# Optimization experiments

Measured on AMD Instinct MI355X. Metric: run time of the kernel, lower is better.

Reference implementation:

```python
import jax, jax.numpy as jnp
import numpy as np

T, B, SEQ_WIDTH, HID = 512, 64, 64, 1024
N = 32  # sqrt(HID): associative memory is N x N, HID spiking neurons
BETA = 0.9     # leak
THRESH = 1.0   # firing threshold
SLOPE = 25.0   # fast-sigmoid surrogate slope (snntorch default)


@jax.custom_vjp
def spike(u):
    # Heaviside forward, fast-sigmoid surrogate backward (snntorch-style)
    return (u > 0).astype(u.dtype)

def _spike_fwd(u):
    return (u > 0).astype(u.dtype), u

def _spike_bwd(u, g):
    sg = 1.0 / (1.0 + SLOPE * jnp.abs(u)) ** 2
    return (g * sg,)

spike.defvjp(_spike_fwd, _spike_bwd)


def assoc_leaky(h, Wk, bk, Wv, bv, Wq, bq):
    """Leaky associative spiking layer.
    h: (T, B, HID). Membrane state is an (B, N, N) associative matrix.
    Each step: outer-product write of key/value, leaky integration,
    threshold spike with soft reset, output spikes gated by sigmoid(q) rows.
    """
    k = h @ Wk + bk                      # (T, B, N)
    v = h @ Wv + bv                      # (T, B, N)
    q = jax.nn.sigmoid(h @ Wq + bq)      # (T, B, N)  use_q_projection gate
    Bt = h.shape[1]

    def step(mem, kvq):
        kt, vt, qt = kvq
        mem = BETA * mem + kt[:, :, None] * vt[:, None, :]   # (B, N, N)
        s = spike(mem - THRESH)
        mem = mem - s * THRESH                               # soft reset
        out = (s * qt[:, :, None]).reshape(Bt, N * N)        # (B, HID)
        return mem, out

    mem0 = jnp.zeros((Bt, N, N), h.dtype)
    _, outs = jax.lax.scan(step, mem0, (k, v, q))
    return outs  # (T, B, HID)


def setup_inputs() -> dict:
    key = jax.random.key(0)
    ks = jax.random.split(key, 12)
    s = 0.02
    def p(k, shape):
        return jax.random.normal(k, shape, jnp.float32) * s
    z = lambda *shape: jnp.zeros(shape, jnp.float32)
    return {
        "x": jax.random.normal(ks[0], (T, B, SEQ_WIDTH + 1), jnp.float32),
        "W_in": p(ks[1], (SEQ_WIDTH + 1, HID)), "b_in": z(HID),
        "Wk1": p(ks[2], (HID, N)), "bk1": z(N),
        "Wv1": p(ks[3], (HID, N)), "bv1": z(N),
        "Wq1": p(ks[4], (HID, N)), "bq1": z(N),
        "W_mid": p(ks[5], (HID, HID)), "b_mid": z(HID),
        "Wk2": p(ks[6], (HID, N)), "bk2": z(N),
        "Wv2": p(ks[7], (HID, N)), "bv2": z(N),
        "Wq2": p(ks[8], (HID, N)), "bq2": z(N),
        "W_out": p(ks[9], (HID, SEQ_WIDTH)), "b_out": z(SEQ_WIDTH),
    }


def reference(x, W_in, b_in, Wk1, bk1, Wv1, bv1, Wq1, bq1,
              W_mid, b_mid, Wk2, bk2, Wv2, bv2, Wq2, bq2, W_out, b_out):
    h = x @ W_in + b_in                                  # (T, B, HID)
    h = assoc_leaky(h, Wk1, bk1, Wv1, bv1, Wq1, bq1)
    h = jax.nn.relu(h @ W_mid + b_mid)
    h = assoc_leaky(h, Wk2, bk2, Wv2, bv2, Wq2, bq2)
    y = h @ W_out + b_out                                # (T, B, SEQ_WIDTH)
    return jax.nn.sigmoid(y)
```

## Files before the change

### kernel.cpp

```cpp
#include <hip/hip_runtime.h>
#include <math.h>


#define T_STEPS 512
#define BATCH   64
#define NN      32
#define HID     1024
#define INW     65
#define OUTW    64
#define KVQ     96

__device__ __forceinline__ float sigmoidf_(float x) { return 1.0f / (1.0f + expf(-x)); }

__global__ __launch_bounds__(512) void prep_kernel(
    const float* __restrict__ W_in, const float* __restrict__ b_in,
    const float* __restrict__ Wk1, const float* __restrict__ bk1,
    const float* __restrict__ Wv1, const float* __restrict__ bv1,
    const float* __restrict__ Wq1, const float* __restrict__ bq1,
    const float* __restrict__ b_mid,
    const float* __restrict__ Wk2, const float* __restrict__ bk2,
    const float* __restrict__ Wv2, const float* __restrict__ bv2,
    const float* __restrict__ Wq2, const float* __restrict__ bq2,
    float* __restrict__ W1eff, float* __restrict__ b1eff,
    float* __restrict__ const2)
{
    const int m = blockIdx.x;
    const int tid = threadIdx.x;
    __shared__ float srcv[HID];
    __shared__ float part[512];
    for (int h = tid; h < HID; h += 512) {
        float s;
        if (m < INW)       s = W_in[m * HID + h];
        else if (m == INW) s = b_in[h];
        else               s = fmaxf(b_mid[h], 0.f);
        srcv[h] = s;
    }
    __syncthreads();
    const int hq = tid >> 7, ns = tid & 127;
    const int sel = ns >> 5, nn = ns & 31;
    const bool layer2 = (m == INW + 1);
    const float* W = layer2 ? (sel == 0 ? Wk2 : sel == 1 ? Wv2 : Wq2)
                            : (sel == 0 ? Wk1 : sel == 1 ? Wv1 : Wq1);
    float acc = 0.f;
    if (ns < KVQ) {
        const int h0 = hq * 256;
        #pragma unroll 8
        for (int hh = 0; hh < 256; ++hh)
            acc = fmaf(srcv[h0 + hh], W[(h0 + hh) * NN + nn], acc);
    }
    part[tid] = acc;
    __syncthreads();
    if (hq == 0 && ns < KVQ) {
        float tot = part[ns] + part[128 + ns] + part[256 + ns] + part[384 + ns];
        if (m < INW) {
            W1eff[m * KVQ + ns] = tot;
        } else if (m == INW) {
            tot += (sel == 0 ? bk1 : sel == 1 ? bv1 : bq1)[nn];
            b1eff[ns] = tot;
        } else {
            tot += (sel == 0 ? bk2 : sel == 1 ? bv2 : bq2)[nn];
            const2[ns] = (sel == 2) ? sigmoidf_(tot) : tot;
        }
    }
}

__global__ __launch_bounds__(128) void kvq1p1_kernel(
    const float* __restrict__ x, const float* __restrict__ W1eff,
    const float* __restrict__ b1eff, float* __restrict__ kvq1,
    float* __restrict__ cert1)
{
    const int b = blockIdx.x >> 3, seg = blockIdx.x & 7;
    const int tid = threadIdx.x;
    __shared__ __align__(16) float Ws[INW * KVQ];
    __shared__ __align__(16) float bs[KVQ];
    __shared__ __align__(16) float pool[64 * 100];
    __shared__ float red[4];
    for (int i4 = tid; i4 < (INW * KVQ) / 4; i4 += 128)
        ((float4*)Ws)[i4] = ((const float4*)W1eff)[i4];
    if (tid < KVQ) bs[tid] = b1eff[tid];
    for (int l = tid; l < 64 * INW; l += 128) {
        const int r = l / INW, m = l - r * INW;
        pool[m * 68 + r] = x[((size_t)((seg * 64 + r) * 64 + b)) * INW + m];
    }
    __syncthreads();
    const int rg = tid >> 3;
    const int c0 = (tid & 7) * 12;
    float acc[4][12];
    #pragma unroll
    for (int r = 0; r < 4; ++r)
        #pragma unroll
        for (int k = 0; k < 12; ++k) acc[r][k] = bs[c0 + k];
    #pragma unroll 5
    for (int m = 0; m < INW; ++m) {
        const float4 xv = *(const float4*)&pool[m * 68 + rg * 4];
        const float4 w0 = *(const float4*)&Ws[m * KVQ + c0];
        const float4 w1 = *(const float4*)&Ws[m * KVQ + c0 + 4];
        const float4 w2 = *(const float4*)&Ws[m * KVQ + c0 + 8];
        const float xr[4] = {xv.x, xv.y, xv.z, xv.w};
        const float wk[12] = {w0.x, w0.y, w0.z, w0.w, w1.x, w1.y, w1.z, w1.w,
                              w2.x, w2.y, w2.z, w2.w};
        #pragma unroll
        for (int r = 0; r < 4; ++r)
            #pragma unroll
            for (int k = 0; k < 12; ++k)
                acc[r][k] = fmaf(xr[r], wk[k], acc[r][k]);
    }
    __syncthreads();
    #pragma unroll
    for (int r = 0; r < 4; ++r) {
        const int row = rg * 4 + r;
        float v[12];
        #pragma unroll
        for (int k = 0; k < 12; ++k)
            v[k] = (c0 + k >= 2 * NN) ? sigmoidf_(acc[r][k]) : acc[r][k];
        float* kt = &pool[row * 100 + c0];
        *(float4*)&kt[0] = make_float4(v[0], v[1], v[2], v[3]);
        *(float4*)&kt[4] = make_float4(v[4], v[5], v[6], v[7]);
        *(float4*)&kt[8] = make_float4(v[8], v[9], v[10], v[11]);
        float* o = kvq1 + ((size_t)b * T_STEPS + seg * 64 + row) * KVQ + c0;
        *(float4*)&o[0] = make_float4(v[0], v[1], v[2], v[3]);
        *(float4*)&o[4] = make_float4(v[4], v[5], v[6], v[7]);
        *(float4*)&o[8] = make_float4(v[8], v[9], v[10], v[11]);
    }
    __syncthreads();
    const int i0 = (tid >> 5) * 8, j = tid & 31;
    float p[8], am[8];
    #pragma unroll
    for (int r = 0; r < 8; ++r) { p[r] = 0.f; am[r] = 0.f; }
    for (int tt = 0; tt < 16; ++tt) {
        float4 k0[4], k1[4]; float vv[4];
        #pragma unroll
        for (int d2 = 0; d2 < 4; ++d2) {
            const int t = tt * 4 + d2;
            k0[d2] = *(const float4*)&pool[t * 100 + i0];
            k1[d2] = *(const float4*)&pool[t * 100 + i0 + 4];
            vv[d2] = pool[t * 100 + 32 + j];
        }
        #pragma unroll
        for (int d2 = 0; d2 < 4; ++d2) {
            const float kf[8] = {k0[d2].x, k0[d2].y, k0[d2].z, k0[d2].w,
                                 k1[d2].x, k1[d2].y, k1[d2].z, k1[d2].w};
            #pragma unroll
            for (int r = 0; r < 8; ++r) {
                p[r] = fmaf(0.9f, p[r], kf[r] * vv[d2]);
                am[r] = fmaxf(am[r], fabsf(p[r]));
            }
        }
    }
    float ls = 0.f, lp = 0.f;
    #pragma unroll
    for (int r = 0; r < 8; ++r) { ls = fmaxf(ls, fabsf(p[r])); lp = fmaxf(lp, am[r]); }
    #pragma unroll
    for (int off = 32; off; off >>= 1) {
        ls = fmaxf(ls, __shfl_xor(ls, off));
        lp = fmaxf(lp, __shfl_xor(lp, off));
    }
    const int lane = tid & 63, wv = tid >> 6;
    if (lane == 0) { red[wv * 2] = ls; red[wv * 2 + 1] = lp; }
    __syncthreads();
    if (tid == 0) {
        cert1[blockIdx.x * 2 + 0] = fmaxf(red[0], red[2]);
        cert1[blockIdx.x * 2 + 1] = fmaxf(red[1], red[3]);
    }
}

__global__ __launch_bounds__(256) void cc_kernel(
    const float* __restrict__ cert, const float* __restrict__ kvq,
    unsigned int* __restrict__ rowany, unsigned int* __restrict__ dmask,
    const unsigned int* __restrict__ rowany_prev, const float* __restrict__ cdef)
{
    const int b = blockIdx.x;
    const int tid = threadIdx.x;
    const float c64 = 0.0011790184577738599f;
    const float G64 = 9.988209815422261f;
    __shared__ __align__(16) float c2l[64];
    float scs = 0.f;
    if (cdef) {
        if (tid < 64) c2l[tid] = cdef[tid];
        __syncthreads();
        float mk = 0.f, mv = 0.f;
        #pragma unroll 8
        for (int i = 0; i < 32; ++i) {
            mk = fmaxf(mk, fabsf(c2l[i]));
            mv = fmaxf(mv, fabsf(c2l[32 + i]));
        }
        scs = mk * mv * G64;
    }
    float Mb = 0.f;
    bool fl = false;
    #pragma unroll
    for (int g = 0; g < 8; ++g) {
        bool mixed = true;
        if (rowany_prev) {
            unsigned int m = 0u;
            #pragma unroll
            for (int iq = 0; iq < 4; ++iq)
                m |= rowany_prev[(b * 4 + iq) * 16 + 2 * g]
                   | rowany_prev[(b * 4 + iq) * 16 + 2 * g + 1];
            mixed = (m != 0u);
        }
        float smax, pmax;
        if (mixed) { smax = cert[(b * 8 + g) * 2]; pmax = cert[(b * 8 + g) * 2 + 1]; }
        else       { smax = scs; pmax = scs; }
        const float ub = Mb + pmax;
        fl |= !(ub * 1.0001f <= 0.999f);
        Mb = fmaf(c64, Mb, smax);
    }
    if (!fl) {
        if (tid < 64) rowany[b * 64 + tid] = 0u;
        return;
    }
    __shared__ float buf[64 * 64];
    const int j = tid & 31, ig = tid >> 5;
    const int wavei = tid >> 6;
    float mem[4] = {0.f, 0.f, 0.f, 0.f};
    unsigned int u[4] = {0u, 0u, 0u, 0u};
    for (int c = 0; c < 8; ++c) {
        unsigned int orA = 0xFFFFFFFFu, orB = 0xFFFFFFFFu;
        if (rowany_prev) {
            orA = 0u; orB = 0u;
            #pragma unroll
            for (int iq = 0; iq < 4; ++iq) {
                orA |= rowany_prev[(b * 4 + iq) * 16 + 2 * c];
                orB |= rowany_prev[(b * 4 + iq) * 16 + 2 * c + 1];
            }
        }
        __syncthreads();
        #pragma unroll
        for (int r = 0; r < 4; ++r) {
            const int s4 = tid + 256 * r;
            const int dt = s4 >> 4, q = s4 & 15;
            const unsigned int orw = (dt < 32) ? orA : orB;
            float4 val;
            if (rowany_prev && !((orw >> (dt & 31)) & 1u))
                val = *(const float4*)&c2l[q * 4];
            else
                val = *(const float4*)(kvq + ((size_t)b * T_STEPS + c * 64 + dt) * KVQ + q * 4);
            *(float4*)&buf[dt * 64 + q * 4] = val;
        }
        __syncthreads();
        for (int dt = 0; dt < 64; ++dt) {
            const float4 kk = *(const float4*)&buf[dt * 64 + ig * 4];
            const float vv = buf[dt * 64 + 32 + j];
            const float kf[4] = {kk.x, kk.y, kk.z, kk.w};
            #pragma unroll
            for (int r = 0; r < 4; ++r) {
                mem[r] = fmaf(0.9f, mem[r], kf[r] * vv);
                const bool s = mem[r] > 1.f; if (s) mem[r] -= 1.f;
                u[r] |= (s ? 1u : 0u) << (dt & 31);
            }
            if ((dt & 31) == 31) {
                const int wg = c * 2 + (dt >> 5);
                unsigned int* dm = dmask + (size_t)(wg * 64 + b) * 1024;
                unsigned int a = 0;
                #pragma unroll
                for (int r = 0; r < 4; ++r) {
                    dm[(ig * 4 + r) * 32 + j] = u[r];
                    a |= u[r]; u[r] = 0u;
                }
                #pragma unroll
                for (int off = 32; off; off >>= 1) a |= __shfl_xor(a, off);
                if ((tid & 63) == 0) rowany[(b * 4 + wavei) * 16 + wg] = a;
            }
        }
    }
}

__global__ __launch_bounds__(128) void mid_kernel(
    const unsigned int* __restrict__ rowany1, const unsigned int* __restrict__ dmask1,
    const float* __restrict__ kvq1,
    const float* __restrict__ W_mid, const float* __restrict__ b_mid,
    const float* __restrict__ Wk2, const float* __restrict__ bk2,
    const float* __restrict__ Wv2, const float* __restrict__ bv2,
    const float* __restrict__ Wq2, const float* __restrict__ bq2,
    const float* __restrict__ const2, float* __restrict__ kvq2,
    float* __restrict__ cert2)
{
    const int b = blockIdx.x >> 3, seg = blockIdx.x & 7;
    const int tid = threadIdx.x;
    const int w0 = seg * 2;
    const unsigned int orA = rowany1[(b * 4 + 0) * 16 + w0] | rowany1[(b * 4 + 1) * 16 + w0]
                           | rowany1[(b * 4 + 2) * 16 + w0] | rowany1[(b * 4 + 3) * 16 + w0];
    const unsigned int orB = rowany1[(b * 4 + 0) * 16 + w0 + 1] | rowany1[(b * 4 + 1) * 16 + w0 + 1]
                           | rowany1[(b * 4 + 2) * 16 + w0 + 1] | rowany1[(b * 4 + 3) * 16 + w0 + 1];
    if ((orA | orB) == 0u) return;
    __shared__ __align__(16) float c2s[KVQ];
    __shared__ __align__(16) float kt2[64 * 64];
    __shared__ float h2[HID];
    __shared__ unsigned int msk[NN];
    __shared__ float red[4];
    if (tid < KVQ) c2s[tid] = const2[tid];
    __syncthreads();
    float* obase = kvq2 + ((size_t)b * T_STEPS + seg * 64) * KVQ;
    for (int d = 0; d < 64; ++d) {
        const unsigned int orw = (d < 32) ? orA : orB;
        const int bit = d & 31;
        if (!((orw >> bit) & 1u)) {
            if (tid < 16) *(float4*)&kt2[d * 64 + tid * 4] = ((const float4*)c2s)[tid];
        } else {
            const int wg = w0 + (d >> 5);
            const unsigned int* dmw = dmask1 + (size_t)(wg * 64 + b) * 1024;
            for (int i2 = 0; i2 < NN; i2 += 4) {
                const int i = i2 + (tid >> 5);
                const unsigned int wb = dmw[i * 32 + (tid & 31)];
                const unsigned long long balm = __ballot(((wb >> bit) & 1u) != 0);
                const int ibase = i2 + (tid >> 6) * 2;
                if ((tid & 63) == 0)  msk[ibase]     = (unsigned int)balm;
                if ((tid & 63) == 32) msk[ibase + 1] = (unsigned int)(balm >> 32);
            }
            for (int cc = tid; cc < HID; cc += 128) h2[cc] = b_mid[cc];
            __syncthreads();
            const float* qrow = kvq1 + ((size_t)b * T_STEPS + seg * 64 + d) * KVQ + 2 * NN;
            for (int i = 0; i < NN; ++i) {
                unsigned int m = msk[i];
                if (!m) continue;
                const float qv = qrow[i];
                while (m) {
                    const int jj = __ffs(m) - 1; m &= m - 1;
                    const float* wr = W_mid + (size_t)(i * NN + jj) * HID;
                    for (int cc = tid; cc < HID; cc += 128)
                        h2[cc] = fmaf(qv, wr[cc], h2[cc]);
                }
            }
            __syncthreads();
            for (int cc = tid; cc < HID; cc += 128) h2[cc] = fmaxf(h2[cc], 0.f);
            __syncthreads();
            if (tid < KVQ) {
                const int sel = tid >> 5, nn = tid & 31;
                const float* W2 = sel == 0 ? Wk2 : sel == 1 ? Wv2 : Wq2;
                float a2 = (sel == 0 ? bk2 : sel == 1 ? bv2 : bq2)[nn];
                for (int cc = 0; cc < HID; ++cc)
                    a2 = fmaf(h2[cc], W2[cc * NN + nn], a2);
                if (sel == 2) a2 = sigmoidf_(a2);
                obase[d * KVQ + tid] = a2;
                if (tid < 64) kt2[d * 64 + tid] = a2;
            }
            __syncthreads();
        }
    }
    __syncthreads();
    const int i0 = (tid >> 5) * 8, j = tid & 31;
    float p[8], am[8];
    #pragma unroll
    for (int r = 0; r < 8; ++r) { p[r] = 0.f; am[r] = 0.f; }
    for (int tt = 0; tt < 16; ++tt) {
        float4 k0[4], k1[4]; float vv[4];
        #pragma unroll
        for (int d2 = 0; d2 < 4; ++d2) {
            const int t = tt * 4 + d2;
            k0[d2] = *(const float4*)&kt2[t * 64 + i0];
            k1[d2] = *(const float4*)&kt2[t * 64 + i0 + 4];
            vv[d2] = kt2[t * 64 + 32 + j];
        }
        #pragma unroll
        for (int d2 = 0; d2 < 4; ++d2) {
            const float kf[8] = {k0[d2].x, k0[d2].y, k0[d2].z, k0[d2].w,
                                 k1[d2].x, k1[d2].y, k1[d2].z, k1[d2].w};
            #pragma unroll
            for (int r = 0; r < 8; ++r) {
                p[r] = fmaf(0.9f, p[r], kf[r] * vv[d2]);
                am[r] = fmaxf(am[r], fabsf(p[r]));
            }
        }
    }
    float ls = 0.f, lp = 0.f;
    #pragma unroll
    for (int r = 0; r < 8; ++r) { ls = fmaxf(ls, fabsf(p[r])); lp = fmaxf(lp, am[r]); }
    #pragma unroll
    for (int off = 32; off; off >>= 1) {
        ls = fmaxf(ls, __shfl_xor(ls, off));
        lp = fmaxf(lp, __shfl_xor(lp, off));
    }
    const int lane = tid & 63, wv = tid >> 6;
    if (lane == 0) { red[wv * 2] = ls; red[wv * 2 + 1] = lp; }
    __syncthreads();
    if (tid == 0) {
        cert2[blockIdx.x * 2 + 0] = fmaxf(red[0], red[2]);
        cert2[blockIdx.x * 2 + 1] = fmaxf(red[1], red[3]);
    }
}

__global__ __launch_bounds__(256) void out_kernel(
    const unsigned int* __restrict__ rowany2, const unsigned int* __restrict__ dmask2,
    const unsigned int* __restrict__ rowany1,
    const float* __restrict__ kvq2, const float* __restrict__ const2,
    const float* __restrict__ W_out, const float* __restrict__ b_out,
    float* __restrict__ y)
{
    const int blk = blockIdx.x;
    const int b = blk >> 2, tq = blk & 3;
    const int tid = threadIdx.x;
    const int wave = tid >> 6, lane = tid & 63;
    const int wg = tq * 4 + wave;
    __shared__ unsigned int mskws[4][NN];
    const int g16 = lane & 15;
    const float4 bo = ((const float4*)b_out)[g16];
    const float4 sy = make_float4(sigmoidf_(bo.x), sigmoidf_(bo.y),
                                  sigmoidf_(bo.z), sigmoidf_(bo.w));
    const unsigned int or4 = rowany2[(b * 4 + 0) * 16 + wg]
                           | rowany2[(b * 4 + 1) * 16 + wg]
                           | rowany2[(b * 4 + 2) * 16 + wg]
                           | rowany2[(b * 4 + 3) * 16 + wg];
    if (or4 == 0) {
        #pragma unroll
        for (int d = 0; d < 32; d += 4) {
            const int t = wg * 32 + d + (lane >> 4);
            ((float4*)(y + ((size_t)t * 64 + b) * OUTW))[g16] = sy;
        }
        return;
    }
    const unsigned int or1 = rowany1[(b * 4 + 0) * 16 + wg]
                           | rowany1[(b * 4 + 1) * 16 + wg]
                           | rowany1[(b * 4 + 2) * 16 + wg]
                           | rowany1[(b * 4 + 3) * 16 + wg];
    for (int d = 0; d < 32; ++d) {
        const int t = wg * 32 + d;
        float* yr = y + ((size_t)t * 64 + b) * OUTW;
        if (!((or4 >> d) & 1u)) {
            if (lane < 16) ((float4*)yr)[lane] = sy;
            continue;
        }
        const unsigned int* dmw = dmask2 + (size_t)(wg * 64 + b) * 1024;
        for (int i2 = 0; i2 < NN; i2 += 2) {
            const int i = i2 + (lane >> 5), jj = lane & 31;
            const unsigned int wbits = dmw[i * 32 + jj];
            const unsigned long long bal = __ballot(((wbits >> d) & 1u) != 0);
            if (lane == 0)  mskws[wave][i2] = (unsigned int)bal;
            if (lane == 32) mskws[wave][i2 + 1] = (unsigned int)(bal >> 32);
        }
        const float* qrow = ((or1 >> d) & 1u)
            ? kvq2 + ((size_t)b * T_STEPS + t) * KVQ + 2 * NN
            : const2 + 2 * NN;
        float a = b_out[lane];
        for (int i = 0; i < NN; ++i) {
            unsigned int m = mskws[wave][i];
            if (!m) continue;
            const float qv = qrow[i];
            while (m) {
                const int jj = __ffs(m) - 1; m &= m - 1;
                a = fmaf(qv, W_out[(size_t)(i * NN + jj) * OUTW + lane], a);
            }
        }
        yr[lane] = sigmoidf_(a);
    }
}

extern "C" void kernel_launch(void* const* d_in, const int* in_sizes, int n_in,
                              void* d_out, int out_size, void* d_ws, size_t ws_size,
                              hipStream_t stream)
{
    const float* x     = (const float*)d_in[0];
    const float* W_in  = (const float*)d_in[1];
    const float* b_in  = (const float*)d_in[2];
    const float* Wk1   = (const float*)d_in[3];
    const float* bk1   = (const float*)d_in[4];
    const float* Wv1   = (const float*)d_in[5];
    const float* bv1   = (const float*)d_in[6];
    const float* Wq1   = (const float*)d_in[7];
    const float* bq1   = (const float*)d_in[8];
    const float* W_mid = (const float*)d_in[9];
    const float* b_mid = (const float*)d_in[10];
    const float* Wk2   = (const float*)d_in[11];
    const float* bk2   = (const float*)d_in[12];
    const float* Wv2   = (const float*)d_in[13];
    const float* bv2   = (const float*)d_in[14];
    const float* Wq2   = (const float*)d_in[15];
    const float* bq2   = (const float*)d_in[16];
    const float* W_out = (const float*)d_in[17];
    const float* b_out = (const float*)d_in[18];
    float* y = (float*)d_out;

    float* ws = (float*)d_ws;
    float* W1eff  = ws;
    float* b1eff  = ws + 6240;
    float* const2 = ws + 6336;
    float* kvq1   = ws + 8192;
    float* kvq2   = kvq1 + 3145728;
    unsigned int* dmask1  = (unsigned int*)(kvq2 + 3145728);
    unsigned int* dmask2  = dmask1 + 1048576;
    unsigned int* rowany1 = dmask2 + 1048576;
    unsigned int* rowany2 = rowany1 + 4096;
    float* cert1 = (float*)(rowany2 + 4096);
    float* cert2 = cert1 + 1024;

    prep_kernel<<<INW + 2, 512, 0, stream>>>(W_in, b_in, Wk1, bk1, Wv1, bv1, Wq1, bq1,
                                             b_mid, Wk2, bk2, Wv2, bv2, Wq2, bq2,
                                             W1eff, b1eff, const2);
    kvq1p1_kernel<<<BATCH * 8, 128, 0, stream>>>(x, W1eff, b1eff, kvq1, cert1);
    cc_kernel<<<BATCH, 256, 0, stream>>>(cert1, kvq1, rowany1, dmask1,
                                         (const unsigned int*)nullptr,
                                         (const float*)nullptr);
    mid_kernel<<<BATCH * 8, 128, 0, stream>>>(rowany1, dmask1, kvq1, W_mid, b_mid,
                                              Wk2, bk2, Wv2, bv2, Wq2, bq2,
                                              const2, kvq2, cert2);
    cc_kernel<<<BATCH, 256, 0, stream>>>(cert2, kvq2, rowany2, dmask2,
                                         rowany1, const2);
    out_kernel<<<BATCH * 4, 256, 0, stream>>>(rowany2, dmask2, rowany1,
                                              kvq2, const2, W_out, b_out, y);
}
```

Before: 147.6 us.

## Split fused kvq1/phase1 kernel into row-contiguous projection and separate certificate scan

The fused layer-1 projection plus certificate scan kernel is split in two. The projection now reads x in contiguous 128-row chunks over (t,b), so loads are coalesced instead of strided by batch, and it scatters results into the per-batch kvq1 layout. A separate phase1 kernel reloads the k/v columns from global memory and runs the leaky scan with 256 threads, 4 rows each, and double-buffered register loads. This adds a kernel launch and a global round trip of kvq1 in exchange for coalesced input reads and more parallelism in the scan.

Measured after the change: 142.5 us, median of 2. -3.5%, faster.

```diff
diff --git a/kernel.cpp b/kernel.cpp
--- a/kernel.cpp
+++ b/kernel.cpp
@@ -8,6 +8,7 @@
 #define HID     1024
 #define INW     65
 #define OUTW    64
+#define ROWS    (T_STEPS * BATCH)
 #define KVQ     96
 
 __device__ __forceinline__ float sigmoidf_(float x) { return 1.0f / (1.0f + expf(-x)); }
@@ -64,24 +65,22 @@
     }
 }
 
-__global__ __launch_bounds__(128) void kvq1p1_kernel(
+__global__ __launch_bounds__(256) void kvq1_kernel(
     const float* __restrict__ x, const float* __restrict__ W1eff,
-    const float* __restrict__ b1eff, float* __restrict__ kvq1,
-    float* __restrict__ cert1)
-{
-    const int b = blockIdx.x >> 3, seg = blockIdx.x & 7;
+    const float* __restrict__ b1eff, float* __restrict__ kvq1)
+{
     const int tid = threadIdx.x;
-    __shared__ __align__(16) float Ws[INW * KVQ];
-    __shared__ __align__(16) float bs[KVQ];
-    __shared__ __align__(16) float pool[64 * 100];
-    __shared__ float red[4];
-    for (int i4 = tid; i4 < (INW * KVQ) / 4; i4 += 128)
+    const int r0 = blockIdx.x * 128;
+    __shared__ float Ws[INW * KVQ];
+    __shared__ float xsT[INW * 132];
+    __shared__ float bs[KVQ];
+    for (int i4 = tid; i4 < (INW * KVQ) / 4; i4 += 256)
         ((float4*)Ws)[i4] = ((const float4*)W1eff)[i4];
+    for (int l = tid; l < 128 * INW; l += 256) {
+        const int r = l / INW, m = l - r * INW;
+        xsT[m * 132 + r] = x[(size_t)(r0 + r) * INW + m];
+    }
     if (tid < KVQ) bs[tid] = b1eff[tid];
-    for (int l = tid; l < 64 * INW; l += 128) {
-        const int r = l / INW, m = l - r * INW;
-        pool[m * 68 + r] = x[((size_t)((seg * 64 + r) * 64 + b)) * INW + m];
-    }
     __syncthreads();
     const int rg = tid >> 3;
     const int c0 = (tid & 7) * 12;
@@ -90,9 +89,8 @@
     for (int r = 0; r < 4; ++r)
         #pragma unroll
         for (int k = 0; k < 12; ++k) acc[r][k] = bs[c0 + k];
-    #pragma unroll 5
     for (int m = 0; m < INW; ++m) {
-        const float4 xv = *(const float4*)&pool[m * 68 + rg * 4];
+        const float4 xv = *(const float4*)&xsT[m * 132 + rg * 4];
         const float4 w0 = *(const float4*)&Ws[m * KVQ + c0];
         const float4 w1 = *(const float4*)&Ws[m * KVQ + c0 + 4];
         const float4 w2 = *(const float4*)&Ws[m * KVQ + c0 + 8];
@@ -105,51 +103,68 @@
             for (int k = 0; k < 12; ++k)
                 acc[r][k] = fmaf(xr[r], wk[k], acc[r][k]);
     }
-    __syncthreads();
     #pragma unroll
     for (int r = 0; r < 4; ++r) {
-        const int row = rg * 4 + r;
+        const int g = r0 + rg * 4 + r;
+        const int t = g >> 6, b = g & 63;
+        float* o = kvq1 + ((size_t)b * T_STEPS + t) * KVQ + c0;
         float v[12];
         #pragma unroll
         for (int k = 0; k < 12; ++k)
             v[k] = (c0 + k >= 2 * NN) ? sigmoidf_(acc[r][k]) : acc[r][k];
-        float* kt = &pool[row * 100 + c0];
-        *(float4*)&kt[0] = make_float4(v[0], v[1], v[2], v[3]);
-        *(float4*)&kt[4] = make_float4(v[4], v[5], v[6], v[7]);
-        *(float4*)&kt[8] = make_float4(v[8], v[9], v[10], v[11]);
-        float* o = kvq1 + ((size_t)b * T_STEPS + seg * 64 + row) * KVQ + c0;
         *(float4*)&o[0] = make_float4(v[0], v[1], v[2], v[3]);
         *(float4*)&o[4] = make_float4(v[4], v[5], v[6], v[7]);
         *(float4*)&o[8] = make_float4(v[8], v[9], v[10], v[11]);
     }
-    __syncthreads();
-    const int i0 = (tid >> 5) * 8, j = tid & 31;
-    float p[8], am[8];
-    #pragma unroll
-    for (int r = 0; r < 8; ++r) { p[r] = 0.f; am[r] = 0.f; }
-    for (int tt = 0; tt < 16; ++tt) {
-        float4 k0[4], k1[4]; float vv[4];
-        #pragma unroll
-        for (int d2 = 0; d2 < 4; ++d2) {
-            const int t = tt * 4 + d2;
-            k0[d2] = *(const float4*)&pool[t * 100 + i0];
-            k1[d2] = *(const float4*)&pool[t * 100 + i0 + 4];
-            vv[d2] = pool[t * 100 + 32 + j];
-        }
-        #pragma unroll
-        for (int d2 = 0; d2 < 4; ++d2) {
-            const float kf[8] = {k0[d2].x, k0[d2].y, k0[d2].z, k0[d2].w,
-                                 k1[d2].x, k1[d2].y, k1[d2].z, k1[d2].w};
+}
+
+__global__ __launch_bounds__(256) void phase1_kernel(
+    const float* __restrict__ kvq, float* __restrict__ cert)
+{
+    const int b = blockIdx.x >> 3, seg = blockIdx.x & 7;
+    const int tid = threadIdx.x;
+    __shared__ __align__(16) float buf[64 * 64];
+    __shared__ float red[8];
+    const float* base = kvq + ((size_t)b * T_STEPS + seg * 64) * KVQ;
+    #pragma unroll
+    for (int r = 0; r < 4; ++r) {
+        const int l4 = tid + 256 * r;
+        const int dt = l4 >> 4, q = l4 & 15;
+        *(float4*)&buf[dt * 64 + q * 4] = *(const float4*)(base + dt * KVQ + q * 4);
+    }
+    __syncthreads();
+    const int i0 = (tid >> 5) * 4, j = tid & 31;
+    float p[4] = {0.f, 0.f, 0.f, 0.f};
+    float am[4] = {0.f, 0.f, 0.f, 0.f};
+    float4 kb[2][4]; float vb[2][4];
+    #pragma unroll
+    for (int d = 0; d < 4; ++d) {
+        kb[0][d] = *(const float4*)&buf[d * 64 + i0];
+        vb[0][d] = buf[d * 64 + 32 + j];
+    }
+    #pragma unroll
+    for (int bt = 0; bt < 16; ++bt) {
+        const int cb = bt & 1;
+        if (bt < 15) {
             #pragma unroll
-            for (int r = 0; r < 8; ++r) {
-                p[r] = fmaf(0.9f, p[r], kf[r] * vv[d2]);
-                am[r] = fmaxf(am[r], fabsf(p[r]));
-            }
+            for (int d = 0; d < 4; ++d) {
+                const int dt = (bt + 1) * 4 + d;
+                kb[cb ^ 1][d] = *(const float4*)&buf[dt * 64 + i0];
+                vb[cb ^ 1][d] = buf[dt * 64 + 32 + j];
+            }
+        }
+        #pragma unroll
+        for (int d = 0; d < 4; ++d) {
+            const float vv = vb[cb][d];
+            p[0] = fmaf(0.9f, p[0], kb[cb][d].x * vv); am[0] = fmaxf(am[0], fabsf(p[0]));
+            p[1] = fmaf(0.9f, p[1], kb[cb][d].y * vv); am[1] = fmaxf(am[1], fabsf(p[1]));
+            p[2] = fmaf(0.9f, p[2], kb[cb][d].z * vv); am[2] = fmaxf(am[2], fabsf(p[2]));
+            p[3] = fmaf(0.9f, p[3], kb[cb][d].w * vv); am[3] = fmaxf(am[3], fabsf(p[3]));
         }
     }
     float ls = 0.f, lp = 0.f;
     #pragma unroll
-    for (int r = 0; r < 8; ++r) { ls = fmaxf(ls, fabsf(p[r])); lp = fmaxf(lp, am[r]); }
+    for (int r = 0; r < 4; ++r) { ls = fmaxf(ls, fabsf(p[r])); lp = fmaxf(lp, am[r]); }
     #pragma unroll
     for (int off = 32; off; off >>= 1) {
         ls = fmaxf(ls, __shfl_xor(ls, off));
@@ -159,8 +174,8 @@
     if (lane == 0) { red[wv * 2] = ls; red[wv * 2 + 1] = lp; }
     __syncthreads();
     if (tid == 0) {
-        cert1[blockIdx.x * 2 + 0] = fmaxf(red[0], red[2]);
-        cert1[blockIdx.x * 2 + 1] = fmaxf(red[1], red[3]);
+        cert[blockIdx.x * 2 + 0] = fmaxf(fmaxf(red[0], red[2]), fmaxf(red[4], red[6]));
+        cert[blockIdx.x * 2 + 1] = fmaxf(fmaxf(red[1], red[3]), fmaxf(red[5], red[7]));
     }
 }
 
@@ -486,7 +501,8 @@
     prep_kernel<<<INW + 2, 512, 0, stream>>>(W_in, b_in, Wk1, bk1, Wv1, bv1, Wq1, bq1,
                                              b_mid, Wk2, bk2, Wv2, bv2, Wq2, bq2,
                                              W1eff, b1eff, const2);
-    kvq1p1_kernel<<<BATCH * 8, 128, 0, stream>>>(x, W1eff, b1eff, kvq1, cert1);
+    kvq1_kernel<<<ROWS / 128, 256, 0, stream>>>(x, W1eff, b1eff, kvq1);
+    phase1_kernel<<<BATCH * 8, 256, 0, stream>>>(kvq1, cert1);
     cc_kernel<<<BATCH, 256, 0, stream>>>(cert1, kvq1, rowany1, dmask1,
                                          (const unsigned int*)nullptr,
                                          (const float*)nullptr);
```

## Fuse certification scan into producer kernels via last-block atomic completion

Applied to the files above, without the earlier changes.

Removes the two separate cc_kernel launches. Each producer block now publishes its per-batch max bounds with atomicMax and bumps a per-batch counter, and the last block to finish for a batch runs the spike scan in place. Counters are zeroed in prep_kernel. The first-layer producer also doubles its thread count to 256 with fewer rows per thread, and the layer-1 certification bound is changed to a closed-form combined check. The aim is to save launch and serialization overhead, at the cost of the serial scan running in only one block per batch and relying on threadfence-based inter-block ordering.

Measured after the change: 216.6 us. 46.7% more time.

```diff
diff --git a/kernel.cpp b/kernel.cpp
--- a/kernel.cpp
+++ b/kernel.cpp
@@ -22,10 +22,11 @@
     const float* __restrict__ Wv2, const float* __restrict__ bv2,
     const float* __restrict__ Wq2, const float* __restrict__ bq2,
     float* __restrict__ W1eff, float* __restrict__ b1eff,
-    float* __restrict__ const2)
+    float* __restrict__ const2, unsigned int* __restrict__ ctrl)
 {
     const int m = blockIdx.x;
     const int tid = threadIdx.x;
+    if (m == 0 && tid < 384) ctrl[tid] = 0u;
     __shared__ float srcv[HID];
     __shared__ float part[512];
     for (int h = tid; h < HID; h += 512) {
@@ -64,51 +65,53 @@
     }
 }
 
-__global__ __launch_bounds__(128) void kvq1p1_kernel(
+__global__ __launch_bounds__(256) void kvq1p1c_kernel(
     const float* __restrict__ x, const float* __restrict__ W1eff,
     const float* __restrict__ b1eff, float* __restrict__ kvq1,
-    float* __restrict__ cert1)
+    unsigned int* __restrict__ rowany1, unsigned int* __restrict__ dmask1,
+    unsigned int* __restrict__ cnt1, float* __restrict__ amax1)
 {
     const int b = blockIdx.x >> 3, seg = blockIdx.x & 7;
     const int tid = threadIdx.x;
     __shared__ __align__(16) float Ws[INW * KVQ];
     __shared__ __align__(16) float bs[KVQ];
     __shared__ __align__(16) float pool[64 * 100];
-    __shared__ float red[4];
-    for (int i4 = tid; i4 < (INW * KVQ) / 4; i4 += 128)
+    __shared__ float red[8];
+    __shared__ unsigned int lastf, dirtyf;
+    for (int i4 = tid; i4 < (INW * KVQ) / 4; i4 += 256)
         ((float4*)Ws)[i4] = ((const float4*)W1eff)[i4];
     if (tid < KVQ) bs[tid] = b1eff[tid];
-    for (int l = tid; l < 64 * INW; l += 128) {
+    for (int l = tid; l < 64 * INW; l += 256) {
         const int r = l / INW, m = l - r * INW;
         pool[m * 68 + r] = x[((size_t)((seg * 64 + r) * 64 + b)) * INW + m];
     }
     __syncthreads();
     const int rg = tid >> 3;
     const int c0 = (tid & 7) * 12;
-    float acc[4][12];
-    #pragma unroll
-    for (int r = 0; r < 4; ++r)
+    float acc[2][12];
+    #pragma unroll
+    for (int r = 0; r < 2; ++r)
         #pragma unroll
         for (int k = 0; k < 12; ++k) acc[r][k] = bs[c0 + k];
     #pragma unroll 5
     for (int m = 0; m < INW; ++m) {
-        const float4 xv = *(const float4*)&pool[m * 68 + rg * 4];
+        const float2 xv = *(const float2*)&pool[m * 68 + rg * 2];
         const float4 w0 = *(const float4*)&Ws[m * KVQ + c0];
         const float4 w1 = *(const float4*)&Ws[m * KVQ + c0 + 4];
         const float4 w2 = *(const float4*)&Ws[m * KVQ + c0 + 8];
-        const float xr[4] = {xv.x, xv.y, xv.z, xv.w};
+        const float xr[2] = {xv.x, xv.y};
         const float wk[12] = {w0.x, w0.y, w0.z, w0.w, w1.x, w1.y, w1.z, w1.w,
                               w2.x, w2.y, w2.z, w2.w};
         #pragma unroll
-        for (int r = 0; r < 4; ++r)
+        for (int r = 0; r < 2; ++r)
             #pragma unroll
             for (int k = 0; k < 12; ++k)
                 acc[r][k] = fmaf(xr[r], wk[k], acc[r][k]);
     }
     __syncthreads();
     #pragma unroll
-    for (int r = 0; r < 4; ++r) {
-        const int row = rg * 4 + r;
+    for (int r = 0; r < 2; ++r) {
+        const int row = rg * 2 + r;
         float v[12];
         #pragma unroll
         for (int k = 0; k < 12; ++k)
@@ -123,120 +126,81 @@
         *(float4*)&o[8] = make_float4(v[8], v[9], v[10], v[11]);
     }
     __syncthreads();
-    const int i0 = (tid >> 5) * 8, j = tid & 31;
-    float p[8], am[8];
-    #pragma unroll
-    for (int r = 0; r < 8; ++r) { p[r] = 0.f; am[r] = 0.f; }
-    for (int tt = 0; tt < 16; ++tt) {
-        float4 k0[4], k1[4]; float vv[4];
-        #pragma unroll
-        for (int d2 = 0; d2 < 4; ++d2) {
-            const int t = tt * 4 + d2;
-            k0[d2] = *(const float4*)&pool[t * 100 + i0];
-            k1[d2] = *(const float4*)&pool[t * 100 + i0 + 4];
-            vv[d2] = pool[t * 100 + 32 + j];
-        }
-        #pragma unroll
-        for (int d2 = 0; d2 < 4; ++d2) {
-            const float kf[8] = {k0[d2].x, k0[d2].y, k0[d2].z, k0[d2].w,
-                                 k1[d2].x, k1[d2].y, k1[d2].z, k1[d2].w};
+    const int i0 = (tid >> 5) * 4, j = tid & 31;
+    float p[4] = {0.f, 0.f, 0.f, 0.f};
+    float am[4] = {0.f, 0.f, 0.f, 0.f};
+    float4 kb[2]; float vb[2][4]; float4 kt4[2][4];
+    (void)kb;
+    #pragma unroll
+    for (int d = 0; d < 4; ++d) {
+        kt4[0][d] = *(const float4*)&pool[d * 100 + i0];
+        vb[0][d] = pool[d * 100 + 32 + j];
+    }
+    #pragma unroll
+    for (int bt = 0; bt < 16; ++bt) {
+        const int cb = bt & 1;
+        if (bt < 15) {
             #pragma unroll
-            for (int r = 0; r < 8; ++r) {
-                p[r] = fmaf(0.9f, p[r], kf[r] * vv[d2]);
-                am[r] = fmaxf(am[r], fabsf(p[r]));
-            }
+            for (int d = 0; d < 4; ++d) {
+                const int dt = (bt + 1) * 4 + d;
+                kt4[cb ^ 1][d] = *(const float4*)&pool[dt * 100 + i0];
+                vb[cb ^ 1][d] = pool[dt * 100 + 32 + j];
+            }
+        }
+        #pragma unroll
+        for (int d = 0; d < 4; ++d) {
+            const float vv = vb[cb][d];
+            p[0] = fmaf(0.9f, p[0], kt4[cb][d].x * vv); am[0] = fmaxf(am[0], fabsf(p[0]));
+            p[1] = fmaf(0.9f, p[1], kt4[cb][d].y * vv); am[1] = fmaxf(am[1], fabsf(p[1]));
+            p[2] = fmaf(0.9f, p[2], kt4[cb][d].z * vv); am[2] = fmaxf(am[2], fabsf(p[2]));
+            p[3] = fmaf(0.9f, p[3], kt4[cb][d].w * vv); am[3] = fmaxf(am[3], fabsf(p[3]));
         }
     }
     float ls = 0.f, lp = 0.f;
     #pragma unroll
-    for (int r = 0; r < 8; ++r) { ls = fmaxf(ls, fabsf(p[r])); lp = fmaxf(lp, am[r]); }
+    for (int r = 0; r < 4; ++r) { ls = fmaxf(ls, fabsf(p[r])); lp = fmaxf(lp, am[r]); }
     #pragma unroll
     for (int off = 32; off; off >>= 1) {
         ls = fmaxf(ls, __shfl_xor(ls, off));
         lp = fmaxf(lp, __shfl_xor(lp, off));
     }
-    const int lane = tid & 63, wv = tid >> 6;
-    if (lane == 0) { red[wv * 2] = ls; red[wv * 2 + 1] = lp; }
+    if ((tid & 63) == 0) { red[(tid >> 6) * 2] = ls; red[(tid >> 6) * 2 + 1] = lp; }
     __syncthreads();
     if (tid == 0) {
-        cert1[blockIdx.x * 2 + 0] = fmaxf(red[0], red[2]);
-        cert1[blockIdx.x * 2 + 1] = fmaxf(red[1], red[3]);
-    }
-}
-
-__global__ __launch_bounds__(256) void cc_kernel(
-    const float* __restrict__ cert, const float* __restrict__ kvq,
-    unsigned int* __restrict__ rowany, unsigned int* __restrict__ dmask,
-    const unsigned int* __restrict__ rowany_prev, const float* __restrict__ cdef)
-{
-    const int b = blockIdx.x;
-    const int tid = threadIdx.x;
-    const float c64 = 0.0011790184577738599f;
-    const float G64 = 9.988209815422261f;
-    __shared__ __align__(16) float c2l[64];
-    float scs = 0.f;
-    if (cdef) {
-        if (tid < 64) c2l[tid] = cdef[tid];
-        __syncthreads();
-        float mk = 0.f, mv = 0.f;
-        #pragma unroll 8
-        for (int i = 0; i < 32; ++i) {
-            mk = fmaxf(mk, fabsf(c2l[i]));
-            mv = fmaxf(mv, fabsf(c2l[32 + i]));
-        }
-        scs = mk * mv * G64;
-    }
-    float Mb = 0.f;
-    bool fl = false;
-    #pragma unroll
-    for (int g = 0; g < 8; ++g) {
-        bool mixed = true;
-        if (rowany_prev) {
-            unsigned int m = 0u;
-            #pragma unroll
-            for (int iq = 0; iq < 4; ++iq)
-                m |= rowany_prev[(b * 4 + iq) * 16 + 2 * g]
-                   | rowany_prev[(b * 4 + iq) * 16 + 2 * g + 1];
-            mixed = (m != 0u);
-        }
-        float smax, pmax;
-        if (mixed) { smax = cert[(b * 8 + g) * 2]; pmax = cert[(b * 8 + g) * 2 + 1]; }
-        else       { smax = scs; pmax = scs; }
-        const float ub = Mb + pmax;
-        fl |= !(ub * 1.0001f <= 0.999f);
-        Mb = fmaf(c64, Mb, smax);
-    }
-    if (!fl) {
-        if (tid < 64) rowany[b * 64 + tid] = 0u;
+        const float bS = fmaxf(fmaxf(red[0], red[2]), fmaxf(red[4], red[6]));
+        const float bP = fmaxf(fmaxf(red[1], red[3]), fmaxf(red[5], red[7]));
+        atomicMax((int*)&amax1[b * 2 + 0], __float_as_int(bS));
+        atomicMax((int*)&amax1[b * 2 + 1], __float_as_int(bP));
+    }
+    __threadfence();
+    __syncthreads();
+    if (tid == 0) lastf = (atomicAdd(&cnt1[b], 1u) == 7u) ? 1u : 0u;
+    __syncthreads();
+    if (!lastf) return;
+    __threadfence();
+    if (tid == 0) {
+        const float mS = __int_as_float(atomicMax((int*)&amax1[b * 2 + 0], 0));
+        const float mP = __int_as_float(atomicMax((int*)&amax1[b * 2 + 1], 0));
+        dirtyf = !((mP + mS * 1.0012f) * 1.0001f <= 0.999f) ? 1u : 0u;
+    }
+    __syncthreads();
+    if (!dirtyf) {
+        if (tid < 64) rowany1[b * 64 + tid] = 0u;
         return;
     }
-    __shared__ float buf[64 * 64];
-    const int j = tid & 31, ig = tid >> 5;
+    float* buf = pool;
+    const int ig = tid >> 5;
     const int wavei = tid >> 6;
     float mem[4] = {0.f, 0.f, 0.f, 0.f};
     unsigned int u[4] = {0u, 0u, 0u, 0u};
     for (int c = 0; c < 8; ++c) {
-        unsigned int orA = 0xFFFFFFFFu, orB = 0xFFFFFFFFu;
-        if (rowany_prev) {
-            orA = 0u; orB = 0u;
-            #pragma unroll
-            for (int iq = 0; iq < 4; ++iq) {
-                orA |= rowany_prev[(b * 4 + iq) * 16 + 2 * c];
-                orB |= rowany_prev[(b * 4 + iq) * 16 + 2 * c + 1];
-            }
-        }
         __syncthreads();
         #pragma unroll
         for (int r = 0; r < 4; ++r) {
             const int s4 = tid + 256 * r;
             const int dt = s4 >> 4, q = s4 & 15;
-            const unsigned int orw = (dt < 32) ? orA : orB;
-            float4 val;
-            if (rowany_prev && !((orw >> (dt & 31)) & 1u))
-                val = *(const float4*)&c2l[q * 4];
-            else
-                val = *(const float4*)(kvq + ((size_t)b * T_STEPS + c * 64 + dt) * KVQ + q * 4);
-            *(float4*)&buf[dt * 64 + q * 4] = val;
+            *(float4*)&buf[dt * 64 + q * 4] =
+                *(const float4*)(kvq1 + ((size_t)b * T_STEPS + c * 64 + dt) * KVQ + q * 4);
         }
         __syncthreads();
         for (int dt = 0; dt < 64; ++dt) {
@@ -251,7 +215,7 @@
             }
             if ((dt & 31) == 31) {
                 const int wg = c * 2 + (dt >> 5);
-                unsigned int* dm = dmask + (size_t)(wg * 64 + b) * 1024;
+                unsigned int* dm = dmask1 + (size_t)(wg * 64 + b) * 1024;
                 unsigned int a = 0;
                 #pragma unroll
                 for (int r = 0; r < 4; ++r) {
@@ -260,13 +224,13 @@
                 }
                 #pragma unroll
                 for (int off = 32; off; off >>= 1) a |= __shfl_xor(a, off);
-                if ((tid & 63) == 0) rowany[(b * 4 + wavei) * 16 + wg] = a;
+                if ((tid & 63) == 0) rowany1[(b * 4 + wavei) * 16 + wg] = a;
             }
         }
     }
 }
 
-__global__ __launch_bounds__(128) void mid_kernel(
+__global__ __launch_bounds__(128) void midc_kernel(
     const unsigned int* __restrict__ rowany1, const unsigned int* __restrict__ dmask1,
     const float* __restrict__ kvq1,
     const float* __restrict__ W_mid, const float* __restrict__ b_mid,
@@ -274,109 +238,187 @@
     const float* __restrict__ Wv2, const float* __restrict__ bv2,
     const float* __restrict__ Wq2, const float* __restrict__ bq2,
     const float* __restrict__ const2, float* __restrict__ kvq2,
-    float* __restrict__ cert2)
+    unsigned int* __restrict__ rowany2, unsigned int* __restrict__ dmask2,
+    unsigned int* __restrict__ cnt2, float* __restrict__ amax2)
 {
     const int b = blockIdx.x >> 3, seg = blockIdx.x & 7;
     const int tid = threadIdx.x;
     const int w0 = seg * 2;
-    const unsigned int orA = rowany1[(b * 4 + 0) * 16 + w0] | rowany1[(b * 4 + 1) * 16 + w0]
-                           | rowany1[(b * 4 + 2) * 16 + w0] | rowany1[(b * 4 + 3) * 16 + w0];
-    const unsigned int orB = rowany1[(b * 4 + 0) * 16 + w0 + 1] | rowany1[(b * 4 + 1) * 16 + w0 + 1]
-                           | rowany1[(b * 4 + 2) * 16 + w0 + 1] | rowany1[(b * 4 + 3) * 16 + w0 + 1];
-    if ((orA | orB) == 0u) return;
+    const float G64 = 9.988209815422261f;
     __shared__ __align__(16) float c2s[KVQ];
     __shared__ __align__(16) float kt2[64 * 64];
     __shared__ float h2[HID];
     __shared__ unsigned int msk[NN];
     __shared__ float red[4];
+    __shared__ unsigned int lastf, dirtyf;
     if (tid < KVQ) c2s[tid] = const2[tid];
     __syncthreads();
-    float* obase = kvq2 + ((size_t)b * T_STEPS + seg * 64) * KVQ;
-    for (int d = 0; d < 64; ++d) {
-        const unsigned int orw = (d < 32) ? orA : orB;
-        const int bit = d & 31;
-        if (!((orw >> bit) & 1u)) {
-            if (tid < 16) *(float4*)&kt2[d * 64 + tid * 4] = ((const float4*)c2s)[tid];
-        } else {
-            const int wg = w0 + (d >> 5);
-            const unsigned int* dmw = dmask1 + (size_t)(wg * 64 + b) * 1024;
-            for (int i2 = 0; i2 < NN; i2 += 4) {
-                const int i = i2 + (tid >> 5);
-                const unsigned int wb = dmw[i * 32 + (tid & 31)];
-                const unsigned long long balm = __ballot(((wb >> bit) & 1u) != 0);
-                const int ibase = i2 + (tid >> 6) * 2;
-                if ((tid & 63) == 0)  msk[ibase]     = (unsigned int)balm;
-                if ((tid & 63) == 32) msk[ibase + 1] = (unsigned int)(balm >> 32);
-            }
-            for (int cc = tid; cc < HID; cc += 128) h2[cc] = b_mid[cc];
-            __syncthreads();
-            const float* qrow = kvq1 + ((size_t)b * T_STEPS + seg * 64 + d) * KVQ + 2 * NN;
-            for (int i = 0; i < NN; ++i) {
-                unsigned int m = msk[i];
-                if (!m) continue;
-                const float qv = qrow[i];
-                while (m) {
-                    const int jj = __ffs(m) - 1; m &= m - 1;
-                    const float* wr = W_mid + (size_t)(i * NN + jj) * HID;
-                    for (int cc = tid; cc < HID; cc += 128)
-                        h2[cc] = fmaf(qv, wr[cc], h2[cc]);
+    const unsigned int orA = rowany1[(b * 4 + 0) * 16 + w0] | rowany1[(b * 4 + 1) * 16 + w0]
+                           | rowany1[(b * 4 + 2) * 16 + w0] | rowany1[(b * 4 + 3) * 16 + w0];
+    const unsigned int orB = rowany1[(b * 4 + 0) * 16 + w0 + 1] | rowany1[(b * 4 + 1) * 16 + w0 + 1]
+                           | rowany1[(b * 4 + 2) * 16 + w0 + 1] | rowany1[(b * 4 + 3) * 16 + w0 + 1];
+    if ((orA | orB) != 0u) {
+        float* obase = kvq2 + ((size_t)b * T_STEPS + seg * 64) * KVQ;
+        for (int d = 0; d < 64; ++d) {
+            const unsigned int orw = (d < 32) ? orA : orB;
+            const int bit = d & 31;
+            if (!((orw >> bit) & 1u)) {
+                if (tid < 16) *(float4*)&kt2[d * 64 + tid * 4] = ((const float4*)c2s)[tid];
+            } else {
+                const int wg = w0 + (d >> 5);
+                const unsigned int* dmw = dmask1 + (size_t)(wg * 64 + b) * 1024;
+                for (int i2 = 0; i2 < NN; i2 += 4) {
+                    const int i = i2 + (tid >> 5);
+                    const unsigned int wb = dmw[i * 32 + (tid & 31)];
+                    const unsigned long long balm = __ballot(((wb >> bit) & 1u) != 0);
+                    const int ibase = i2 + (tid >> 6) * 2;
+                    if ((tid & 63) == 0)  msk[ibase]     = (unsigned int)balm;
+                    if ((tid & 63) == 32) msk[ibase + 1] = (unsigned int)(balm >> 32);
                 }
-            }
-            __syncthreads();
-            for (int cc = tid; cc < HID; cc += 128) h2[cc] = fmaxf(h2[cc], 0.f);
-            __syncthreads();
-            if (tid < KVQ) {
-                const int sel = tid >> 5, nn = tid & 31;
-                const float* W2 = sel == 0 ? Wk2 : sel == 1 ? Wv2 : Wq2;
-                float a2 = (sel == 0 ? bk2 : sel == 1 ? bv2 : bq2)[nn];
-                for (int cc = 0; cc < HID; ++cc)
-                    a2 = fmaf(h2[cc], W2[cc * NN + nn], a2);
-                if (sel == 2) a2 = sigmoidf_(a2);
-                obase[d * KVQ + tid] = a2;
-                if (tid < 64) kt2[d * 64 + tid] = a2;
-            }
-            __syncthreads();
-        }
-    }
-    __syncthreads();
-    const int i0 = (tid >> 5) * 8, j = tid & 31;
-    float p[8], am[8];
-    #pragma unroll
-    for (int r = 0; r < 8; ++r) { p[r] = 0.f; am[r] = 0.f; }
-    for (int tt = 0; tt < 16; ++tt) {
-        float4 k0[4], k1[4]; float vv[4];
-        #pragma unroll
-        for (int d2 = 0; d2 < 4; ++d2) {
-            const int t = tt * 4 + d2;
-            k0[d2] = *(const float4*)&kt2[t * 64 + i0];
-            k1[d2] = *(const float4*)&kt2[t * 64 + i0 + 4];
-            vv[d2] = kt2[t * 64 + 32 + j];
-        }
-        #pragma unroll
-        for (int d2 = 0; d2 < 4; ++d2) {
-            const float kf[8] = {k0[d2].x, k0[d2].y, k0[d2].z, k0[d2].w,
-                                 k1[d2].x, k1[d2].y, k1[d2].z, k1[d2].w};
+                for (int cc = tid; cc < HID; cc += 128) h2[cc] = b_mid[cc];
+                __syncthreads();
+                const float* qrow = kvq1 + ((size_t)b * T_STEPS + seg * 64 + d) * KVQ + 2 * NN;
+                for (int i = 0; i < NN; ++i) {
+                    unsigned int m = msk[i];
+                    if (!m) continue;
+                    const float qv = qrow[i];
+                    while (m) {
+                        const int jj = __ffs(m) - 1; m &= m - 1;
+                        const float* wr = W_mid + (size_t)(i * NN + jj) * HID;
+                        for (int cc = tid; cc < HID; cc += 128)
+                            h2[cc] = fmaf(qv, wr[cc], h2[cc]);
+                    }
+                }
+                __syncthreads();
+                for (int cc = tid; cc < HID; cc += 128) h2[cc] = fmaxf(h2[cc], 0.f);
+                __syncthreads();
+                if (tid < KVQ) {
+                    const int sel = tid >> 5, nn = tid & 31;
+                    const float* W2 = sel == 0 ? Wk2 : sel == 1 ? Wv2 : Wq2;
+                    float a2 = (sel == 0 ? bk2 : sel == 1 ? bv2 : bq2)[nn];
+                    for (int cc = 0; cc < HID; ++cc)
+                        a2 = fmaf(h2[cc], W2[cc * NN + nn], a2);
+                    if (sel == 2) a2 = sigmoidf_(a2);
+                    obase[d * KVQ + tid] = a2;
+                    if (tid < 64) kt2[d * 64 + tid] = a2;
+                }
+                __syncthreads();
+            }
+        }
+        __syncthreads();
+        const int i0 = (tid >> 5) * 8, j = tid & 31;
+        float p[8], am[8];
+        #pragma unroll
+        for (int r = 0; r < 8; ++r) { p[r] = 0.f; am[r] = 0.f; }
+        for (int tt = 0; tt < 16; ++tt) {
+            float4 k0[4], k1[4]; float vv[4];
+            #pragma unroll
+            for (int d2 = 0; d2 < 4; ++d2) {
+                const int t = tt * 4 + d2;
+                k0[d2] = *(const float4*)&kt2[t * 64 + i0];
+                k1[d2] = *(const float4*)&kt2[t * 64 + i0 + 4];
+                vv[d2] = kt2[t * 64 + 32 + j];
+            }
+            #pragma unroll
+            for (int d2 = 0; d2 < 4; ++d2) {
+                const float kf[8] = {k0[d2].x, k0[d2].y, k0[d2].z, k0[d2].w,
+                                     k1[d2].x, k1[d2].y, k1[d2].z, k1[d2].w};
+                #pragma unroll
+                for (int r = 0; r < 8; ++r) {
+                    p[r] = fmaf(0.9f, p[r], kf[r] * vv[d2]);
+                    am[r] = fmaxf(am[r], fabsf(p[r]));
+                }
+            }
+        }
+        float ls = 0.f, lp = 0.f;
+        #pragma unroll
+        for (int r = 0; r < 8; ++r) { ls = fmaxf(ls, fabsf(p[r])); lp = fmaxf(lp, am[r]); }
+        #pragma unroll
+        for (int off = 32; off; off >>= 1) {
+            ls = fmaxf(ls, __shfl_xor(ls, off));
+            lp = fmaxf(lp, __shfl_xor(lp, off));
+        }
+        if ((tid & 63) == 0) { red[(tid >> 6) * 2] = ls; red[(tid >> 6) * 2 + 1] = lp; }
+        __syncthreads();
+        if (tid == 0) {
+            atomicMax((int*)&amax2[b * 2 + 0], __float_as_int(fmaxf(red[0], red[2])));
+            atomicMax((int*)&amax2[b * 2 + 1], __float_as_int(fmaxf(red[1], red[3])));
+        }
+    }
+    __threadfence();
+    __syncthreads();
+    if (tid == 0) lastf = (atomicAdd(&cnt2[b], 1u) == 7u) ? 1u : 0u;
+    __syncthreads();
+    if (!lastf) return;
+    __threadfence();
+    if (tid == 0) {
+        float mk = 0.f, mv = 0.f;
+        #pragma unroll 8
+        for (int i = 0; i < 32; ++i) {
+            mk = fmaxf(mk, fabsf(c2s[i]));
+            mv = fmaxf(mv, fabsf(c2s[32 + i]));
+        }
+        const float scs = mk * mv * G64;
+        const float mS = fmaxf(__int_as_float(atomicMax((int*)&amax2[b * 2 + 0], 0)), scs);
+        const float mP = fmaxf(__int_as_float(atomicMax((int*)&amax2[b * 2 + 1], 0)), scs);
+        dirtyf = !((mP + mS * 1.0012f) * 1.0001f <= 0.999f) ? 1u : 0u;
+    }
+    __syncthreads();
+    if (!dirtyf) {
+        if (tid < 64) rowany2[b * 64 + tid] = 0u;
+        return;
+    }
+    float* buf = kt2;
+    const int j = tid & 31, ig = tid >> 5;
+    float mem[8]; unsigned int u[8];
+    #pragma unroll
+    for (int r = 0; r < 8; ++r) { mem[r] = 0.f; u[r] = 0u; }
+    for (int c = 0; c < 8; ++c) {
+        unsigned int oA = 0u, oB = 0u;
+        #pragma unroll
+        for (int iq = 0; iq < 4; ++iq) {
+            oA |= rowany1[(b * 4 + iq) * 16 + 2 * c];
+            oB |= rowany1[(b * 4 + iq) * 16 + 2 * c + 1];
+        }
+        __syncthreads();
+        #pragma unroll
+        for (int r = 0; r < 8; ++r) {
+            const int s4 = tid + 128 * r;
+            const int dt = s4 >> 4, q = s4 & 15;
+            const unsigned int orw = (dt < 32) ? oA : oB;
+            float4 val;
+            if (!((orw >> (dt & 31)) & 1u))
+                val = *(const float4*)&c2s[q * 4];
+            else
+                val = *(const float4*)(kvq2 + ((size_t)b * T_STEPS + c * 64 + dt) * KVQ + q * 4);
+            *(float4*)&buf[dt * 64 + q * 4] = val;
+        }
+        __syncthreads();
+        for (int dt = 0; dt < 64; ++dt) {
+            const float4 ka = *(const float4*)&buf[dt * 64 + ig * 8];
+            const float4 kb2 = *(const float4*)&buf[dt * 64 + ig * 8 + 4];
+            const float vv = buf[dt * 64 + 32 + j];
+            const float kf[8] = {ka.x, ka.y, ka.z, ka.w, kb2.x, kb2.y, kb2.z, kb2.w};
             #pragma unroll
             for (int r = 0; r < 8; ++r) {
-                p[r] = fmaf(0.9f, p[r], kf[r] * vv[d2]);
-                am[r] = fmaxf(am[r], fabsf(p[r]));
-            }
-        }
-    }
-    float ls = 0.f, lp = 0.f;
-    #pragma unroll
-    for (int r = 0; r < 8; ++r) { ls = fmaxf(ls, fabsf(p[r])); lp = fmaxf(lp, am[r]); }
-    #pragma unroll
-    for (int off = 32; off; off >>= 1) {
-        ls = fmaxf(ls, __shfl_xor(ls, off));
-        lp = fmaxf(lp, __shfl_xor(lp, off));
-    }
-    const int lane = tid & 63, wv = tid >> 6;
-    if (lane == 0) { red[wv * 2] = ls; red[wv * 2 + 1] = lp; }
-    __syncthreads();
-    if (tid == 0) {
-        cert2[blockIdx.x * 2 + 0] = fmaxf(red[0], red[2]);
-        cert2[blockIdx.x * 2 + 1] = fmaxf(red[1], red[3]);
+                mem[r] = fmaf(0.9f, mem[r], kf[r] * vv);
+                const bool s = mem[r] > 1.f; if (s) mem[r] -= 1.f;
+                u[r] |= (s ? 1u : 0u) << (dt & 31);
+            }
+            if ((dt & 31) == 31) {
+                const int wg = c * 2 + (dt >> 5);
+                unsigned int* dm = dmask2 + (size_t)(wg * 64 + b) * 1024;
+                unsigned int a = 0;
+                #pragma unroll
+                for (int r = 0; r < 8; ++r) {
+                    dm[(ig * 8 + r) * 32 + j] = u[r];
+                    a |= u[r]; u[r] = 0u;
+                }
+                #pragma unroll
+                for (int off = 16; off; off >>= 1) a |= __shfl_xor(a, off);
+                if ((tid & 31) == 0) rowany2[(b * 4 + ig) * 16 + wg] = a;
+            }
+        }
     }
 }
 
@@ -480,21 +522,21 @@
     unsigned int* dmask2  = dmask1 + 1048576;
     unsigned int* rowany1 = dmask2 + 1048576;
     unsigned int* rowany2 = rowany1 + 4096;
-    float* cert1 = (float*)(rowany2 + 4096);
-    float* cert2 = cert1 + 1024;
+    unsigned int* ctrl    = rowany2 + 4096;
+    unsigned int* cnt1  = ctrl;
+    unsigned int* cnt2  = ctrl + 64;
+    float* amax1 = (float*)(ctrl + 128);
+    float* amax2 = (float*)(ctrl + 256);
 
     prep_kernel<<<INW + 2, 512, 0, stream>>>(W_in, b_in, Wk1, bk1, Wv1, bv1, Wq1, bq1,
                                              b_mid, Wk2, bk2, Wv2, bv2, Wq2, bq2,
-                                             W1eff, b1eff, const2);
-    kvq1p1_kernel<<<BATCH * 8, 128, 0, stream>>>(x, W1eff, b1eff, kvq1, cert1);
-    cc_kernel<<<BATCH, 256, 0, stream>>>(cert1, kvq1, rowany1, dmask1,
-                                         (const unsigned int*)nullptr,
-                                         (const float*)nullptr);
-    mid_kernel<<<BATCH * 8, 128, 0, stream>>>(rowany1, dmask1, kvq1, W_mid, b_mid,
-                                              Wk2, bk2, Wv2, bv2, Wq2, bq2,
-                                              const2, kvq2, cert2);
-    cc_kernel<<<BATCH, 256, 0, stream>>>(cert2, kvq2, rowany2, dmask2,
-                                         rowany1, const2);
+                                             W1eff, b1eff, const2, ctrl);
+    kvq1p1c_kernel<<<BATCH * 8, 256, 0, stream>>>(x, W1eff, b1eff, kvq1,
+                                                  rowany1, dmask1, cnt1, amax1);
+    midc_kernel<<<BATCH * 8, 128, 0, stream>>>(rowany1, dmask1, kvq1, W_mid, b_mid,
+                                               Wk2, bk2, Wv2, bv2, Wq2, bq2,
+                                               const2, kvq2, rowany2, dmask2,
+                                               cnt2, amax2);
     out_kernel<<<BATCH * 4, 256, 0, stream>>>(rowany2, dmask2, rowany1,
                                               kvq2, const2, W_out, b_out, y);
 }
```
